# Kernel optimization log

Measured on AMD Instinct MI355X. Metric: run time of the kernel, lower is better.

## Reference

```python
import jax, jax.numpy as jnp
import numpy as np

USER_NUM = 120000
ITEM_NUM = 80000
N_NODES = USER_NUM + ITEM_NUM
N_EDGES = 3200000
EMBED_DIM = 64
GNN_LAYERS = 3


def setup_inputs() -> dict:
    key = jax.random.key(0)
    k1, k2, k3, k4, k5 = jax.random.split(key, 5)
    user_embeds = jax.random.normal(k1, (USER_NUM, EMBED_DIM), dtype=jnp.float32)
    item_embeds = jax.random.normal(k2, (ITEM_NUM, EMBED_DIM), dtype=jnp.float32)
    rows = jax.random.randint(k3, (N_EDGES,), 0, N_NODES, dtype=jnp.int32)
    cols = jax.random.randint(k4, (N_EDGES,), 0, N_NODES, dtype=jnp.int32)
    vals = jax.random.uniform(k5, (N_EDGES,), dtype=jnp.float32)
    return {"user_embeds": user_embeds, "item_embeds": item_embeds,
            "rows": rows, "cols": cols, "vals": vals}


def _spmm(rows, cols, vals, embeds):
    # sparse adj (COO) @ dense embeds: out[r] += v * embeds[c]
    msgs = vals[:, None] * embeds[cols]          # [E, D]
    return jax.ops.segment_sum(msgs, rows, num_segments=N_NODES)


def reference(user_embeds, item_embeds, rows, cols, vals):
    embeds = jnp.concatenate([user_embeds, item_embeds], axis=0)  # [N, D]
    pooled = embeds  # 'sum' pooling accumulates layer 0
    for _ in range(GNN_LAYERS):
        embeds = _spmm(rows, cols, vals, embeds)
        pooled = pooled + embeds
    return pooled[:USER_NUM], pooled[USER_NUM:]
```

## Files before the change

kernel.cpp:

```cpp
#include <hip/hip_runtime.h>
#include <hip/hip_fp16.h>

#define USER_NUM 120000
#define ITEM_NUM 80000
#define N_NODES (USER_NUM + ITEM_NUM)
#define N_EDGES 3200000
#define D 64
#define BSHIFT 8
#define BROWS 256
#define N_BUCKETS ((N_NODES + BROWS - 1) >> BSHIFT)
#define BPAD 5120
#define SCATTER_CHUNK 4096
#define COL_MASK 0x3FFFF

__global__ void init_kernel(const float* __restrict__ user,
                            const float* __restrict__ item,
                            __half* __restrict__ L0) {
    const int total4 = N_NODES * D / 4;
    const int user4  = USER_NUM * D / 4;
    int idx = blockIdx.x * blockDim.x + threadIdx.x;
    const int stride = gridDim.x * blockDim.x;
    const float4* u4 = (const float4*)user;
    const float4* i4 = (const float4*)item;
    float2* o2 = (float2*)L0;
    for (; idx < total4; idx += stride) {
        float4 v = (idx < user4) ? u4[idx] : i4[idx - user4];
        union { __half2 h[2]; float2 f; } u;
        u.h[0] = __floats2half2_rn(v.x, v.y);
        u.h[1] = __floats2half2_rn(v.z, v.w);
        o2[idx] = u.f;
    }
}

__global__ void scatter_kernel(const int* __restrict__ rows,
                               const int* __restrict__ cols,
                               const float* __restrict__ vals,
                               int* __restrict__ bcursor,
                               int2* __restrict__ cv_tmp) {
    __shared__ int cnt[N_BUCKETS];
    __shared__ int gb[N_BUCKETS];
    const int t = threadIdx.x;
    for (int cbase = blockIdx.x * SCATTER_CHUNK; cbase < N_EDGES;
         cbase += gridDim.x * SCATTER_CHUNK) {
        const int cend = min(cbase + SCATTER_CHUNK, N_EDGES);
        for (int i = t; i < N_BUCKETS; i += 256) cnt[i] = 0;
        __syncthreads();
        for (int e = cbase + t; e < cend; e += 256)
            atomicAdd(&cnt[rows[e] >> BSHIFT], 1);
        __syncthreads();
        for (int i = t; i < N_BUCKETS; i += 256) {
            const int c = cnt[i];
            gb[i] = c ? atomicAdd(&bcursor[i], c) : 0;
            cnt[i] = 0;
        }
        __syncthreads();
        for (int e = cbase + t; e < cend; e += 256) {
            const int r = rows[e];
            const int b = r >> BSHIFT;
            const int off = atomicAdd(&cnt[b], 1);
            cv_tmp[(size_t)b * BPAD + gb[b] + off] =
                make_int2(((r & (BROWS - 1)) << 18) | cols[e], __float_as_int(vals[e]));
        }
        __syncthreads();
    }
}

__global__ void rowsort_kernel(const int* __restrict__ bcursor,
                               const int2* __restrict__ cv_tmp,
                               int2* __restrict__ cv,
                               int2* __restrict__ row_se) {
    __shared__ int hist[BROWS];
    __shared__ int sstart[BROWS];
    __shared__ int cursor[BROWS];
    const int b = blockIdx.x;
    const int t = threadIdx.x;
    const int base = b * BPAD;
    const int count = bcursor[b];
    hist[t] = 0;
    __syncthreads();
    for (int e = t; e < count; e += 256)
        atomicAdd(&hist[(cv_tmp[base + e].x >> 18) & (BROWS - 1)], 1);
    __syncthreads();
    if (t < 64) {
        int carry = 0;
        for (int bb = 0; bb < BROWS; bb += 64) {
            const int x = hist[bb + t];
            int v = x;
            #pragma unroll
            for (int d = 1; d < 64; d <<= 1) {
                int y = __shfl_up(v, d);
                if (t >= d) v += y;
            }
            sstart[bb + t] = carry + v - x;
            carry += __shfl(v, 63);
        }
    }
    __syncthreads();
    cursor[t] = sstart[t];
    const int grow = (b << BSHIFT) + t;
    if (grow < N_NODES)
        row_se[grow] = make_int2(base + sstart[t], base + sstart[t] + hist[t]);
    __syncthreads();
    for (int e = t; e < count; e += 256) {
        const int2 p = cv_tmp[base + e];
        const int lr = (p.x >> 18) & (BROWS - 1);
        const int pos = base + atomicAdd(&cursor[lr], 1);
        cv[pos] = make_int2(p.x & COL_MASK, p.y);
    }
}

__global__ __launch_bounds__(256) void spmm_kernel(const int2* __restrict__ row_se,
                                                   const int2* __restrict__ cv,
                                                   const __half* __restrict__ in,
                                                   __half* __restrict__ out,
                                                   const __half* __restrict__ P0,
                                                   const __half* __restrict__ P1,
                                                   float* __restrict__ pooled,
                                                   int last) {
    const int row = (blockIdx.x * blockDim.x + threadIdx.x) >> 4;
    const int l   = threadIdx.x & 15;
    if (row >= N_NODES) return;
    const int2 se = row_se[row];
    float a0 = 0.f, a1 = 0.f, a2 = 0.f, a3 = 0.f;
    for (int e = se.x; e < se.y; e += 4) {
        #pragma unroll
        for (int u = 0; u < 4; ++u) {
            const int ee = e + u;
            const bool valid = ee < se.y;
            const int2 p = cv[valid ? ee : se.x];
            const float v = valid ? __int_as_float(p.y) : 0.f;
            const float2 raw = *(const float2*)&in[((size_t)p.x << 6) + (l << 2)];
            union { float2 f; __half2 h[2]; } q; q.f = raw;
            const float2 x0 = __half22float2(q.h[0]);
            const float2 x1 = __half22float2(q.h[1]);
            a0 = fmaf(v, x0.x, a0); a1 = fmaf(v, x0.y, a1);
            a2 = fmaf(v, x1.x, a2); a3 = fmaf(v, x1.y, a3);
        }
    }
    const size_t off = ((size_t)row << 6) + (l << 2);
    if (!last) {
        union { float2 f; __half2 h[2]; } o;
        o.h[0] = __floats2half2_rn(a0, a1);
        o.h[1] = __floats2half2_rn(a2, a3);
        *(float2*)&out[off] = o.f;
    } else {
        union { float2 f; __half2 h[2]; } q0, q1, q2;
        q0.f = *(const float2*)&P0[off];
        q1.f = *(const float2*)&P1[off];
        q2.f = *(const float2*)&in[off];
        const float2 s00 = __half22float2(q0.h[0]), s01 = __half22float2(q0.h[1]);
        const float2 s10 = __half22float2(q1.h[0]), s11 = __half22float2(q1.h[1]);
        const float2 s20 = __half22float2(q2.h[0]), s21 = __half22float2(q2.h[1]);
        *(float4*)&pooled[off] = make_float4(a0 + s00.x + s10.x + s20.x,
                                             a1 + s00.y + s10.y + s20.y,
                                             a2 + s01.x + s11.x + s21.x,
                                             a3 + s01.y + s11.y + s21.y);
    }
}

extern "C" void kernel_launch(void* const* d_in, const int* in_sizes, int n_in,
                              void* d_out, int out_size, void* d_ws, size_t ws_size,
                              hipStream_t stream) {
    const float* user = (const float*)d_in[0];
    const float* item = (const float*)d_in[1];
    const int*   rows = (const int*)d_in[2];
    const int*   cols = (const int*)d_in[3];
    const float* vals = (const float*)d_in[4];

    float* pooled = (float*)d_out;

    char* p = (char*)d_ws;
    const size_t embB = (size_t)N_NODES * D * 2;
    __half* L0 = (__half*)p;  p += embB;
    __half* L1 = (__half*)p;  p += embB;
    __half* L2 = (__half*)p;  p += embB;
    int2* cv_tmp = (int2*)L1;
    int2* cv     = (int2*)p;   p += (size_t)N_BUCKETS * BPAD * 8;
    int2* row_se = (int2*)p;   p += (size_t)N_NODES * 8;
    int*  bcursor = (int*)p;   p += (size_t)N_BUCKETS * 4;

    const dim3 blk256(256);
    hipMemsetAsync(bcursor, 0, (size_t)N_BUCKETS * 4, stream);

    init_kernel<<<2048, blk256, 0, stream>>>(user, item, L0);
    scatter_kernel<<<(N_EDGES + SCATTER_CHUNK - 1) / SCATTER_CHUNK, blk256, 0, stream>>>(
        rows, cols, vals, bcursor, cv_tmp);
    rowsort_kernel<<<N_BUCKETS, blk256, 0, stream>>>(bcursor, cv_tmp, cv, row_se);

    const dim3 grid_spmm((N_NODES * 16 + 255) / 256);
    spmm_kernel<<<grid_spmm, blk256, 0, stream>>>(row_se, cv, L0, L1, nullptr, nullptr, nullptr, 0);
    spmm_kernel<<<grid_spmm, blk256, 0, stream>>>(row_se, cv, L1, L2, nullptr, nullptr, nullptr, 0);
    spmm_kernel<<<grid_spmm, blk256, 0, stream>>>(row_se, cv, L2, nullptr, L0, L1, pooled, 1);
}
```

Measured before the change: 515.1 us.

## Stage scatter output in shared memory for coalesced writes; unroll SpMM by 8

The scatter kernel now counts edges per bucket, computes local bucket offsets with a wavefront prefix scan, and sorts each chunk's edges into shared memory by bucket. It then writes them to the global bucket arrays in bucket order, so writes to the same bucket land contiguously instead of scattering per edge. The cost is roughly 40KB of extra shared memory per block, which lowers occupancy. Separately, the SpMM inner loop unroll goes from 4 to 8 to keep more gathers in flight, at the cost of more wasted padded iterations on short rows.

```diff
diff --git a/kernel.cpp b/kernel.cpp
--- a/kernel.cpp
+++ b/kernel.cpp
@@ -32,34 +32,59 @@
     }
 }
 
-__global__ void scatter_kernel(const int* __restrict__ rows,
-                               const int* __restrict__ cols,
-                               const float* __restrict__ vals,
-                               int* __restrict__ bcursor,
-                               int2* __restrict__ cv_tmp) {
+__global__ __launch_bounds__(256) void scatter_kernel(const int* __restrict__ rows,
+                                                      const int* __restrict__ cols,
+                                                      const float* __restrict__ vals,
+                                                      int* __restrict__ bcursor,
+                                                      int2* __restrict__ cv_tmp) {
     __shared__ int cnt[N_BUCKETS];
-    __shared__ int gb[N_BUCKETS];
+    __shared__ int lstart[N_BUCKETS];
+    __shared__ int gbase[N_BUCKETS];
+    __shared__ int2 stage[SCATTER_CHUNK];
+    __shared__ unsigned short sbucket[SCATTER_CHUNK];
     const int t = threadIdx.x;
     for (int cbase = blockIdx.x * SCATTER_CHUNK; cbase < N_EDGES;
          cbase += gridDim.x * SCATTER_CHUNK) {
-        const int cend = min(cbase + SCATTER_CHUNK, N_EDGES);
+        const int csize = min(SCATTER_CHUNK, N_EDGES - cbase);
         for (int i = t; i < N_BUCKETS; i += 256) cnt[i] = 0;
         __syncthreads();
-        for (int e = cbase + t; e < cend; e += 256)
-            atomicAdd(&cnt[rows[e] >> BSHIFT], 1);
+        for (int e = t; e < csize; e += 256)
+            atomicAdd(&cnt[rows[cbase + e] >> BSHIFT], 1);
         __syncthreads();
         for (int i = t; i < N_BUCKETS; i += 256) {
             const int c = cnt[i];
-            gb[i] = c ? atomicAdd(&bcursor[i], c) : 0;
-            cnt[i] = 0;
-        }
-        __syncthreads();
-        for (int e = cbase + t; e < cend; e += 256) {
-            const int r = rows[e];
+            gbase[i] = c ? atomicAdd(&bcursor[i], c) : 0;
+        }
+        if (t < 64) {
+            int carry = 0;
+            for (int base = 0; base < N_BUCKETS; base += 64) {
+                const int i = base + t;
+                const int x = (i < N_BUCKETS) ? cnt[i] : 0;
+                int v = x;
+                #pragma unroll
+                for (int d = 1; d < 64; d <<= 1) {
+                    int y = __shfl_up(v, d);
+                    if (t >= d) v += y;
+                }
+                if (i < N_BUCKETS) lstart[i] = carry + v - x;
+                carry += __shfl(v, 63);
+            }
+        }
+        __syncthreads();
+        for (int i = t; i < N_BUCKETS; i += 256) cnt[i] = lstart[i];
+        __syncthreads();
+        for (int e = t; e < csize; e += 256) {
+            const int r = rows[cbase + e];
             const int b = r >> BSHIFT;
             const int off = atomicAdd(&cnt[b], 1);
-            cv_tmp[(size_t)b * BPAD + gb[b] + off] =
-                make_int2(((r & (BROWS - 1)) << 18) | cols[e], __float_as_int(vals[e]));
+            stage[off] = make_int2(((r & (BROWS - 1)) << 18) | cols[cbase + e],
+                                   __float_as_int(vals[cbase + e]));
+            sbucket[off] = (unsigned short)b;
+        }
+        __syncthreads();
+        for (int i = t; i < csize; i += 256) {
+            const int b = sbucket[i];
+            cv_tmp[(size_t)b * BPAD + gbase[b] + (i - lstart[b])] = stage[i];
         }
         __syncthreads();
     }
@@ -122,9 +147,9 @@
     if (row >= N_NODES) return;
     const int2 se = row_se[row];
     float a0 = 0.f, a1 = 0.f, a2 = 0.f, a3 = 0.f;
-    for (int e = se.x; e < se.y; e += 4) {
+    for (int e = se.x; e < se.y; e += 8) {
         #pragma unroll
-        for (int u = 0; u < 4; ++u) {
+        for (int u = 0; u < 8; ++u) {
             const int ee = e + u;
             const bool valid = ee < se.y;
             const int2 p = cv[valid ? ee : se.x];
```

New measurement: 503.8 us. 2.2% less time.
